# Kernel tuning notes

Hardware: AMD Instinct MI355X
Metric: run time of the kernel (lower is better)

Reference implementation:

```python
import jax, jax.numpy as jnp
import numpy as np

N_NODES = 100000
IN_DIM = 128
HID_DIM = 128
OUT_DIM = 3
N_EDGES = 1600000


def gcn_conv(x, W, b, src, dst, num_nodes):
    """PyG GCNConv: x' = D^{-1/2}(A+I)D^{-1/2} (x W) + b, where (src,dst) already include self-loops."""
    xw = x @ W                                        # [N, out]
    deg = jax.ops.segment_sum(jnp.ones_like(dst, dtype=xw.dtype), dst, num_segments=num_nodes)
    dinv = jax.lax.rsqrt(jnp.maximum(deg, 1.0))        # deg >= 1 due to self-loops
    norm = dinv[src] * dinv[dst]                       # [E]
    msg = xw[src] * norm[:, None]                      # gather  [E, out]
    out = jax.ops.segment_sum(msg, dst, num_segments=num_nodes)  # scatter-add [N, out]
    return out + b


def setup_inputs() -> dict:
    key = jax.random.key(0)
    k1, k2, k3, k4, k5 = jax.random.split(key, 5)
    feature = jax.random.normal(k1, (N_NODES, IN_DIM), dtype=jnp.float32)
    edge_index = jax.random.randint(k2, (2, N_EDGES), 0, N_NODES, dtype=jnp.int32)
    edge_type = jax.random.randint(k3, (N_EDGES,), 0, 2, dtype=jnp.int32)
    W1 = jax.random.normal(k4, (IN_DIM, HID_DIM), dtype=jnp.float32) / np.sqrt(IN_DIM)
    b1 = jnp.zeros((HID_DIM,), dtype=jnp.float32)
    W2 = jax.random.normal(k5, (HID_DIM, OUT_DIM), dtype=jnp.float32) / np.sqrt(HID_DIM)
    b2 = jnp.zeros((OUT_DIM,), dtype=jnp.float32)
    return {"feature": feature, "edge_index": edge_index, "edge_type": edge_type,
            "W1": W1, "b1": b1, "W2": W2, "b2": b2}


def reference(feature, edge_index, edge_type, W1, b1, W2, b2):
    n = feature.shape[0]
    loops = jnp.arange(n, dtype=edge_index.dtype)
    src = jnp.concatenate([edge_index[0], loops])   # add self-loops once, reused by both layers
    dst = jnp.concatenate([edge_index[1], loops])
    x = jax.nn.relu(gcn_conv(feature, W1, b1, src, dst, n))
    # dropout is identity at inference (training=False)
    x = gcn_conv(x, W2, b2, src, dst, n)
    return x
```

## Files before the change

kernel.cpp:

```cpp
#include <hip/hip_runtime.h>
#include <hip/hip_fp16.h>

#define N_NODES 100000
#define N_EDGES 1600000
#define D 128
#define NBKT 391
#define BKT_CAP 5120
#define NB_GEMM 3125
#define NB_BINA 782


__global__ __launch_bounds__(512) void mega_kernel(const float* __restrict__ x,
                                                   const float* __restrict__ W,
                                                   float* __restrict__ xw,
                                                   const int* __restrict__ src,
                                                   const int* __restrict__ dst,
                                                   int* __restrict__ gcnt,
                                                   int* __restrict__ staged) {
    __shared__ __align__(16) char smem[81920];
    const int tid = threadIdx.x;
    const int bid = blockIdx.x;

    if (bid < NB_GEMM) {
        float* ws_ = (float*)smem;
        float* xs_ = (float*)smem + 16384;
        float4* ws4 = (float4*)ws_;
        const float4* W4 = (const float4*)W;
#pragma unroll
        for (int i = 0; i < 8; ++i) ws4[tid + i * 512] = W4[tid + i * 512];
        const int row0 = bid * 32;
        const float4* x4 = (const float4*)(x + (size_t)row0 * D);
        float4* xs4 = (float4*)xs_;
        xs4[tid] = x4[tid];
        xs4[tid + 512] = x4[tid + 512];
        __syncthreads();
        const int rg = tid >> 5;
        const int c0 = (tid & 31) * 4;
        float acc0[4] = {0, 0, 0, 0}, acc1[4] = {0, 0, 0, 0};
#pragma unroll 8
        for (int k = 0; k < D; ++k) {
            const float4 wv = *(const float4*)&ws_[k * D + c0];
            const float xv0 = xs_[rg * D + k];
            const float xv1 = xs_[(rg + 16) * D + k];
            acc0[0] += xv0 * wv.x; acc0[1] += xv0 * wv.y;
            acc0[2] += xv0 * wv.z; acc0[3] += xv0 * wv.w;
            acc1[0] += xv1 * wv.x; acc1[1] += xv1 * wv.y;
            acc1[2] += xv1 * wv.z; acc1[3] += xv1 * wv.w;
        }
        *(float4*)&xw[(size_t)(row0 + rg) * D + c0] = *(float4*)acc0;
        *(float4*)&xw[(size_t)(row0 + rg + 16) * D + c0] = *(float4*)acc1;
    } else {
        int* hist = (int*)smem;
        if (tid < NBKT) hist[tid] = 0;
        __syncthreads();
        const int i4 = (bid - NB_GEMM) * 512 + tid;
        const bool valid = i4 < N_EDGES / 4;
        int4 dv, sv;
        int lb0 = 0, lb1 = 0, lb2 = 0, lb3 = 0, lr0 = 0, lr1 = 0, lr2 = 0, lr3 = 0;
        if (valid) {
            dv = ((const int4*)dst)[i4];
            sv = ((const int4*)src)[i4];
            lb0 = dv.x >> 8; lr0 = atomicAdd(&hist[lb0], 1);
            lb1 = dv.y >> 8; lr1 = atomicAdd(&hist[lb1], 1);
            lb2 = dv.z >> 8; lr2 = atomicAdd(&hist[lb2], 1);
            lb3 = dv.w >> 8; lr3 = atomicAdd(&hist[lb3], 1);
        }
        __syncthreads();
        if (tid < NBKT) {
            const int c = hist[tid];
            hist[tid] = c ? atomicAdd(&gcnt[tid], c) : 0;
        }
        __syncthreads();
        if (valid) {
            staged[lb0 * BKT_CAP + hist[lb0] + lr0] = (sv.x << 8) | (dv.x & 255);
            staged[lb1 * BKT_CAP + hist[lb1] + lr1] = (sv.y << 8) | (dv.y & 255);
            staged[lb2 * BKT_CAP + hist[lb2] + lr2] = (sv.z << 8) | (dv.z & 255);
            staged[lb3 * BKT_CAP + hist[lb3] + lr3] = (sv.w << 8) | (dv.w & 255);
        }
    }
}


__global__ __launch_bounds__(256) void binB_kernel(const int* __restrict__ gcnt,
                                                   const int* __restrict__ staged,
                                                   int* __restrict__ row_ptr,
                                                   int* __restrict__ esrc,
                                                   float* __restrict__ dinv) {
    __shared__ int red[256];
    __shared__ int hist[256];
    __shared__ int nbase[256];
    __shared__ int nexc[256];
    const int b = blockIdx.x;
    const int t = threadIdx.x;
    const int m = gcnt[b];
    int partial = 0;
    for (int i = t; i < b; i += 256) partial += gcnt[i];
    red[t] = partial;
    __syncthreads();
    for (int off = 128; off; off >>= 1) {
        if (t < off) red[t] += red[t + off];
        __syncthreads();
    }
    const int bbase = red[0];
    hist[t] = 0;
    __syncthreads();
    const int* reg = staged + (size_t)b * BKT_CAP;
    for (int i = t; i < m; i += 256) atomicAdd(&hist[reg[i] & 255], 1);
    __syncthreads();
    const int v = hist[t];
    nbase[t] = v;
    __syncthreads();
    for (int off = 1; off < 256; off <<= 1) {
        int u = (t >= off) ? nbase[t - off] : 0;
        __syncthreads();
        nbase[t] += u;
        __syncthreads();
    }
    nexc[t] = nbase[t] - v;
    const int node = b * 256 + t;
    if (node < N_NODES) {
        row_ptr[node] = bbase + nexc[t];
        dinv[node] = rsqrtf((float)v + 1.0f);
    }
    if (b == 0 && t == 0) row_ptr[N_NODES] = N_EDGES;
    hist[t] = 0;
    __syncthreads();
    for (int i = t; i < m; i += 256) {
        const int rec = reg[i];
        const int nl = rec & 255;
        const int r = atomicAdd(&hist[nl], 1);
        esrc[bbase + nexc[nl] + r] = rec >> 8;
    }
}


__global__ __launch_bounds__(256) void qscale_kernel(const float* __restrict__ xw,
                                                     const float* __restrict__ dinv,
                                                     uint4* __restrict__ q4) {
    const int i = blockIdx.x * blockDim.x + threadIdx.x;
    const int n = i >> 4;
    const float dn = dinv[n];
    const float4 a = *(const float4*)&xw[(size_t)i * 8];
    const float4 b = *(const float4*)&xw[(size_t)i * 8 + 4];
    union { uint4 u; __half h[8]; } o;
    o.h[0] = __float2half(a.x * dn); o.h[1] = __float2half(a.y * dn);
    o.h[2] = __float2half(a.z * dn); o.h[3] = __float2half(a.w * dn);
    o.h[4] = __float2half(b.x * dn); o.h[5] = __float2half(b.y * dn);
    o.h[6] = __float2half(b.z * dn); o.h[7] = __float2half(b.w * dn);
    q4[i] = o.u;
}


__global__ __launch_bounds__(256) void gather1_kernel(const int* __restrict__ row_ptr,
                                                      const int* __restrict__ esrc,
                                                      const float* __restrict__ dinv,
                                                      const uint4* __restrict__ q4,
                                                      const float* __restrict__ b1,
                                                      const float* __restrict__ W2,
                                                      float* __restrict__ y) {
    const int t = threadIdx.x;
    const int n = blockIdx.x * 16 + (t >> 4);
    const int g = t & 15;
    const int beg = row_ptr[n], end = row_ptr[n + 1];
    float acc[8] = {0, 0, 0, 0, 0, 0, 0, 0};
    union U { uint4 u; __half2 h2[4]; };
    int j = beg;
    for (; j + 1 < end; j += 2) {
        const int s0 = esrc[j];
        const int s1 = esrc[j + 1];
        U u0, u1;
        u0.u = q4[(size_t)s0 * 16 + g];
        u1.u = q4[(size_t)s1 * 16 + g];
#pragma unroll
        for (int k = 0; k < 4; ++k) {
            const float2 f0 = __half22float2(u0.h2[k]);
            const float2 f1 = __half22float2(u1.h2[k]);
            acc[2 * k + 0] += f0.x + f1.x;
            acc[2 * k + 1] += f0.y + f1.y;
        }
    }
    if (j < end) {
        U u0; u0.u = q4[(size_t)esrc[j] * 16 + g];
#pragma unroll
        for (int k = 0; k < 4; ++k) {
            const float2 f0 = __half22float2(u0.h2[k]);
            acc[2 * k + 0] += f0.x;
            acc[2 * k + 1] += f0.y;
        }
    }
    const float dn = dinv[n];
    U un; un.u = q4[(size_t)n * 16 + g];
    const float4 ba = ((const float4*)b1)[g * 2];
    const float4 bb = ((const float4*)b1)[g * 2 + 1];
    float h[8];
#pragma unroll
    for (int k = 0; k < 4; ++k) {
        const float2 fn = __half22float2(un.h2[k]);
        h[2 * k + 0] = acc[2 * k + 0] + fn.x;
        h[2 * k + 1] = acc[2 * k + 1] + fn.y;
    }
    h[0] = fmaxf(h[0] * dn + ba.x, 0.f); h[1] = fmaxf(h[1] * dn + ba.y, 0.f);
    h[2] = fmaxf(h[2] * dn + ba.z, 0.f); h[3] = fmaxf(h[3] * dn + ba.w, 0.f);
    h[4] = fmaxf(h[4] * dn + bb.x, 0.f); h[5] = fmaxf(h[5] * dn + bb.y, 0.f);
    h[6] = fmaxf(h[6] * dn + bb.z, 0.f); h[7] = fmaxf(h[7] * dn + bb.w, 0.f);
    const int c = g * 8;
    float a0 = 0.f, a1 = 0.f, a2 = 0.f;
#pragma unroll
    for (int k = 0; k < 8; ++k) {
        a0 += h[k] * W2[(c + k) * 3 + 0];
        a1 += h[k] * W2[(c + k) * 3 + 1];
        a2 += h[k] * W2[(c + k) * 3 + 2];
    }
#pragma unroll
    for (int off = 8; off; off >>= 1) {
        a0 += __shfl_xor(a0, off);
        a1 += __shfl_xor(a1, off);
        a2 += __shfl_xor(a2, off);
    }
    if (g == 0) {
        y[n * 3 + 0] = a0 * dn;
        y[n * 3 + 1] = a1 * dn;
        y[n * 3 + 2] = a2 * dn;
    }
}


__global__ __launch_bounds__(256) void gather2_kernel(const int* __restrict__ row_ptr,
                                                      const int* __restrict__ esrc,
                                                      const float* __restrict__ dinv,
                                                      const float* __restrict__ y,
                                                      const float* __restrict__ b2,
                                                      float* __restrict__ out) {
    const int t = threadIdx.x;
    const int node = blockIdx.x * 64 + (t >> 2);
    if (node >= N_NODES) return;
    const int sub = t & 3;
    const int beg = row_ptr[node], end = row_ptr[node + 1];
    float a0 = 0.f, a1 = 0.f, a2 = 0.f;
    for (int j = beg + sub; j < end; j += 4) {
        const int s = esrc[j];
        a0 += y[s * 3 + 0];
        a1 += y[s * 3 + 1];
        a2 += y[s * 3 + 2];
    }
    a0 += __shfl_xor(a0, 1); a0 += __shfl_xor(a0, 2);
    a1 += __shfl_xor(a1, 1); a1 += __shfl_xor(a1, 2);
    a2 += __shfl_xor(a2, 1); a2 += __shfl_xor(a2, 2);
    if (sub == 0) {
        const float dn = dinv[node];
        out[node * 3 + 0] = (a0 + y[node * 3 + 0]) * dn + b2[0];
        out[node * 3 + 1] = (a1 + y[node * 3 + 1]) * dn + b2[1];
        out[node * 3 + 2] = (a2 + y[node * 3 + 2]) * dn + b2[2];
    }
}


extern "C" void kernel_launch(void* const* d_in, const int* in_sizes, int n_in,
                              void* d_out, int out_size, void* d_ws, size_t ws_size,
                              hipStream_t stream) {
    const float* feature = (const float*)d_in[0];
    const int* edge_index = (const int*)d_in[1];
    const int* src = edge_index;
    const int* dst = edge_index + N_EDGES;
    const float* W1 = (const float*)d_in[3];
    const float* b1 = (const float*)d_in[4];
    const float* W2 = (const float*)d_in[5];
    const float* b2 = (const float*)d_in[6];
    float* out = (float*)d_out;

    const size_t ND = (size_t)N_NODES * D;
    float* xw1     = (float*)d_ws;
    uint4* q4      = (uint4*)(xw1 + ND);
    float* y       = (float*)(q4 + (size_t)N_NODES * 16);
    float* dinv    = y + (size_t)N_NODES * 3;
    int*   row_ptr = (int*)(dinv + N_NODES);
    int*   esrc    = row_ptr + (N_NODES + 1);
    int*   gcnt    = esrc + N_EDGES;
    int*   staged  = gcnt + NBKT;

    hipMemsetAsync(gcnt, 0, NBKT * sizeof(int), stream);
    mega_kernel<<<NB_GEMM + NB_BINA, 512, 0, stream>>>(feature, W1, xw1, src, dst, gcnt, staged);
    binB_kernel<<<NBKT, 256, 0, stream>>>(gcnt, staged, row_ptr, esrc, dinv);
    qscale_kernel<<<N_NODES * 16 / 256, 256, 0, stream>>>(xw1, dinv, q4);
    gather1_kernel<<<N_NODES / 16, 256, 0, stream>>>(row_ptr, esrc, dinv, q4, b1, W2, y);
    gather2_kernel<<<(N_NODES + 63) / 64, 256, 0, stream>>>(row_ptr, esrc, dinv, y, b2, out);
}
```

Before: 268.7 us.

## Use fp16 MFMA for layer-1 GEMM, emit fp16 directly, drop qscale pass

The scalar fp32 GEMM is replaced with fp16 MFMA 16x16x32 on a swizzled shared-memory copy of W, and the result is written straight to an fp16 buffer. The separate qscale kernel, which reread the fp32 xw and scaled it by dinv, is removed. The per-source dinv scaling moves into the gather, which now loads dinv[src] per edge. This saves an fp32 write and read of the N×128 intermediate and one launch. In exchange, x and W are rounded to fp16 before the multiply, and the gather does an extra random load and multiply per edge.

```diff
diff --git a/kernel.cpp b/kernel.cpp
--- a/kernel.cpp
+++ b/kernel.cpp
@@ -6,49 +6,86 @@
 #define D 128
 #define NBKT 391
 #define BKT_CAP 5120
-#define NB_GEMM 3125
+#define NB_GEMM 782
 #define NB_BINA 782
+
+typedef _Float16 f16x8 __attribute__((ext_vector_type(8)));
+typedef float f32x4 __attribute__((ext_vector_type(4)));
+
+#define SWZ(b) ((b) ^ ((((b) >> 8) & 7) << 4))
 
 
 __global__ __launch_bounds__(512) void mega_kernel(const float* __restrict__ x,
                                                    const float* __restrict__ W,
-                                                   float* __restrict__ xw,
+                                                   _Float16* __restrict__ q,
                                                    const int* __restrict__ src,
                                                    const int* __restrict__ dst,
                                                    int* __restrict__ gcnt,
                                                    int* __restrict__ staged) {
-    __shared__ __align__(16) char smem[81920];
+    __shared__ __align__(16) char smem[32768];
     const int tid = threadIdx.x;
     const int bid = blockIdx.x;
 
     if (bid < NB_GEMM) {
-        float* ws_ = (float*)smem;
-        float* xs_ = (float*)smem + 16384;
-        float4* ws4 = (float4*)ws_;
-        const float4* W4 = (const float4*)W;
-#pragma unroll
-        for (int i = 0; i < 8; ++i) ws4[tid + i * 512] = W4[tid + i * 512];
-        const int row0 = bid * 32;
-        const float4* x4 = (const float4*)(x + (size_t)row0 * D);
-        float4* xs4 = (float4*)xs_;
-        xs4[tid] = x4[tid];
-        xs4[tid + 512] = x4[tid + 512];
-        __syncthreads();
-        const int rg = tid >> 5;
-        const int c0 = (tid & 31) * 4;
-        float acc0[4] = {0, 0, 0, 0}, acc1[4] = {0, 0, 0, 0};
-#pragma unroll 8
-        for (int k = 0; k < D; ++k) {
-            const float4 wv = *(const float4*)&ws_[k * D + c0];
-            const float xv0 = xs_[rg * D + k];
-            const float xv1 = xs_[(rg + 16) * D + k];
-            acc0[0] += xv0 * wv.x; acc0[1] += xv0 * wv.y;
-            acc0[2] += xv0 * wv.z; acc0[3] += xv0 * wv.w;
-            acc1[0] += xv1 * wv.x; acc1[1] += xv1 * wv.y;
-            acc1[2] += xv1 * wv.z; acc1[3] += xv1 * wv.w;
-        }
-        *(float4*)&xw[(size_t)(row0 + rg) * D + c0] = *(float4*)acc0;
-        *(float4*)&xw[(size_t)(row0 + rg + 16) * D + c0] = *(float4*)acc1;
+        const int lane = tid & 63;
+        const int w = tid >> 6;
+        const int r16 = lane & 15;
+        const int g = lane >> 4;
+        const int row0 = bid * 128;
+        const int row = row0 + w * 16 + r16;
+        const int rowc = row < N_NODES ? row : N_NODES - 1;
+        const float* xp = x + (size_t)rowc * D;
+        f16x8 a[4];
+#pragma unroll
+        for (int kt = 0; kt < 4; ++kt) {
+            const float4 lo = *(const float4*)(xp + kt * 32 + g * 8);
+            const float4 hi = *(const float4*)(xp + kt * 32 + g * 8 + 4);
+            f16x8 v;
+            v[0] = (_Float16)lo.x; v[1] = (_Float16)lo.y; v[2] = (_Float16)lo.z; v[3] = (_Float16)lo.w;
+            v[4] = (_Float16)hi.x; v[5] = (_Float16)hi.y; v[6] = (_Float16)hi.z; v[7] = (_Float16)hi.w;
+            a[kt] = v;
+        }
+        {
+            const int n = tid & 127;
+            const int k0 = (tid >> 7) * 32;
+#pragma unroll
+            for (int c = 0; c < 4; ++c) {
+                f16x8 v;
+#pragma unroll
+                for (int j = 0; j < 8; ++j) v[j] = (_Float16)W[(k0 + c * 8 + j) * D + n];
+                const int byte = n * 256 + (k0 + c * 8) * 2;
+                *(f16x8*)(smem + SWZ(byte)) = v;
+            }
+        }
+        __syncthreads();
+        f32x4 acc[8];
+#pragma unroll
+        for (int nt = 0; nt < 8; ++nt) {
+            f32x4 c = {0.f, 0.f, 0.f, 0.f};
+#pragma unroll
+            for (int kt = 0; kt < 4; ++kt) {
+                const int byte = (nt * 16 + r16) * 256 + kt * 64 + g * 16;
+                const f16x8 b = *(const f16x8*)(smem + SWZ(byte));
+                c = __builtin_amdgcn_mfma_f32_16x16x32_f16(a[kt], b, c, 0, 0, 0);
+            }
+            acc[nt] = c;
+        }
+        __syncthreads();
+        _Float16* qs = (_Float16*)smem;
+#pragma unroll
+        for (int nt = 0; nt < 8; ++nt)
+#pragma unroll
+            for (int r = 0; r < 4; ++r)
+                qs[(w * 16 + g * 4 + r) * D + nt * 16 + r16] = (_Float16)acc[nt][r];
+        __syncthreads();
+        uint4* qg = (uint4*)q;
+#pragma unroll
+        for (int i = 0; i < 4; ++i) {
+            const int c16 = tid + i * 512;
+            const int grow = row0 + (c16 >> 4);
+            if (grow < N_NODES)
+                qg[(size_t)grow * 16 + (c16 & 15)] = *(const uint4*)(smem + c16 * 16);
+        }
     } else {
         int* hist = (int*)smem;
         if (tid < NBKT) hist[tid] = 0;
@@ -131,23 +168,6 @@
         const int r = atomicAdd(&hist[nl], 1);
         esrc[bbase + nexc[nl] + r] = rec >> 8;
     }
-}
-
-
-__global__ __launch_bounds__(256) void qscale_kernel(const float* __restrict__ xw,
-                                                     const float* __restrict__ dinv,
-                                                     uint4* __restrict__ q4) {
-    const int i = blockIdx.x * blockDim.x + threadIdx.x;
-    const int n = i >> 4;
-    const float dn = dinv[n];
-    const float4 a = *(const float4*)&xw[(size_t)i * 8];
-    const float4 b = *(const float4*)&xw[(size_t)i * 8 + 4];
-    union { uint4 u; __half h[8]; } o;
-    o.h[0] = __float2half(a.x * dn); o.h[1] = __float2half(a.y * dn);
-    o.h[2] = __float2half(a.z * dn); o.h[3] = __float2half(a.w * dn);
-    o.h[4] = __float2half(b.x * dn); o.h[5] = __float2half(b.y * dn);
-    o.h[6] = __float2half(b.z * dn); o.h[7] = __float2half(b.w * dn);
-    q4[i] = o.u;
 }
 
 
@@ -168,6 +188,8 @@
     for (; j + 1 < end; j += 2) {
         const int s0 = esrc[j];
         const int s1 = esrc[j + 1];
+        const float d0 = dinv[s0];
+        const float d1 = dinv[s1];
         U u0, u1;
         u0.u = q4[(size_t)s0 * 16 + g];
         u1.u = q4[(size_t)s1 * 16 + g];
@@ -175,17 +197,19 @@
         for (int k = 0; k < 4; ++k) {
             const float2 f0 = __half22float2(u0.h2[k]);
             const float2 f1 = __half22float2(u1.h2[k]);
-            acc[2 * k + 0] += f0.x + f1.x;
-            acc[2 * k + 1] += f0.y + f1.y;
+            acc[2 * k + 0] += f0.x * d0 + f1.x * d1;
+            acc[2 * k + 1] += f0.y * d0 + f1.y * d1;
         }
     }
     if (j < end) {
-        U u0; u0.u = q4[(size_t)esrc[j] * 16 + g];
+        const int s = esrc[j];
+        const float ds = dinv[s];
+        U u0; u0.u = q4[(size_t)s * 16 + g];
 #pragma unroll
         for (int k = 0; k < 4; ++k) {
             const float2 f0 = __half22float2(u0.h2[k]);
-            acc[2 * k + 0] += f0.x;
-            acc[2 * k + 1] += f0.y;
+            acc[2 * k + 0] += f0.x * ds;
+            acc[2 * k + 1] += f0.y * ds;
         }
     }
     const float dn = dinv[n];
@@ -196,8 +220,8 @@
 #pragma unroll
     for (int k = 0; k < 4; ++k) {
         const float2 fn = __half22float2(un.h2[k]);
-        h[2 * k + 0] = acc[2 * k + 0] + fn.x;
-        h[2 * k + 1] = acc[2 * k + 1] + fn.y;
+        h[2 * k + 0] = acc[2 * k + 0] + fn.x * dn;
+        h[2 * k + 1] = acc[2 * k + 1] + fn.y * dn;
     }
     h[0] = fmaxf(h[0] * dn + ba.x, 0.f); h[1] = fmaxf(h[1] * dn + ba.y, 0.f);
     h[2] = fmaxf(h[2] * dn + ba.z, 0.f); h[3] = fmaxf(h[3] * dn + ba.w, 0.f);
@@ -269,9 +293,8 @@
     float* out = (float*)d_out;
 
     const size_t ND = (size_t)N_NODES * D;
-    float* xw1     = (float*)d_ws;
-    uint4* q4      = (uint4*)(xw1 + ND);
-    float* y       = (float*)(q4 + (size_t)N_NODES * 16);
+    _Float16* q    = (_Float16*)d_ws;
+    float* y       = (float*)(q + ND);
     float* dinv    = y + (size_t)N_NODES * 3;
     int*   row_ptr = (int*)(dinv + N_NODES);
     int*   esrc    = row_ptr + (N_NODES + 1);
@@ -279,9 +302,8 @@
     int*   staged  = gcnt + NBKT;
 
     hipMemsetAsync(gcnt, 0, NBKT * sizeof(int), stream);
-    mega_kernel<<<NB_GEMM + NB_BINA, 512, 0, stream>>>(feature, W1, xw1, src, dst, gcnt, staged);
+    mega_kernel<<<NB_GEMM + NB_BINA, 512, 0, stream>>>(feature, W1, q, src, dst, gcnt, staged);
     binB_kernel<<<NBKT, 256, 0, stream>>>(gcnt, staged, row_ptr, esrc, dinv);
-    qscale_kernel<<<N_NODES * 16 / 256, 256, 0, stream>>>(xw1, dinv, q4);
-    gather1_kernel<<<N_NODES / 16, 256, 0, stream>>>(row_ptr, esrc, dinv, q4, b1, W2, y);
+    gather1_kernel<<<N_NODES / 16, 256, 0, stream>>>(row_ptr, esrc, dinv, (const uint4*)q, b1, W2, y);
     gather2_kernel<<<(N_NODES + 63) / 64, 256, 0, stream>>>(row_ptr, esrc, dinv, y, b2, out);
 }
```

Measured after the change: 222.1 us. -17.3%, faster.
